# Optimization experiments

Hardware: AMD Instinct MI355X
Metric: run time of the kernel (lower is better)

## Reference

```python
import jax, jax.numpy as jnp
import numpy as np

BN_SCALE = 1.0 / np.sqrt(1.0 + 1e-5)  # eval BatchNorm with running stats (0,1), gamma=1, beta=0


def fps(xyz, npoint):
    """Farthest point sampling. xyz: [B,N,3] -> int32 indices [B,npoint]. First pick is index 0 (as in pointnet2 CUDA)."""
    xyz = jax.lax.stop_gradient(xyz)  # output is integer indices; non-differentiable
    B, N, _ = xyz.shape

    def step(carry, _):
        dist, last = carry
        p = jnp.take_along_axis(xyz, last[:, None, None], axis=1)  # [B,1,3]
        d = jnp.sum((xyz - p) ** 2, axis=-1)                        # [B,N]
        dist = jnp.minimum(dist, d)
        nxt = jnp.argmax(dist, axis=-1).astype(jnp.int32)
        return (dist, nxt), nxt

    dist0 = jnp.full((B, N), 1e10, dtype=jnp.float32)
    first = jnp.zeros((B,), dtype=jnp.int32)
    _, rest = jax.lax.scan(step, (dist0, first), None, length=npoint - 1)  # [npoint-1, B]
    return jnp.concatenate([first[None, :], rest], axis=0).T  # [B, npoint]


def ball_query(xyz, new_xyz, radius, nsample):
    """For each center pick first nsample point indices with squared dist < radius^2; pad with first hit."""
    xyz = jax.lax.stop_gradient(xyz)
    new_xyz = jax.lax.stop_gradient(new_xyz)
    # expanded squared distance avoids materializing [B,S,N,3]
    d2 = (jnp.sum(new_xyz ** 2, -1)[:, :, None] + jnp.sum(xyz ** 2, -1)[:, None, :]
          - 2.0 * jnp.einsum('bsc,bnc->bsn', new_xyz, xyz))  # [B,S,N]
    N = xyz.shape[1]
    key = jnp.where(d2 < radius * radius, jnp.arange(N, dtype=jnp.int32)[None, None, :], N)
    idx = jnp.sort(key, axis=-1)[..., :nsample]          # first hits in index order
    return jnp.where(idx == N, idx[..., :1], idx)        # pad misses with first hit (center is always a hit)


_gather = jax.vmap(lambda p, i: p[i])  # points [N,C], idx [...] -> [..., C], batched over B


def _mlp(h, params):
    # pointwise Conv2d(1x1) + eval-BN + ReLU stack
    for w, b in params:
        h = jax.nn.relu((h @ w + b) * BN_SCALE)
    return h


def _sa(xyz, feats, npoint, nsample, radius, params):
    ci = fps(xyz, npoint)                               # [B,S]
    new_xyz = _gather(xyz, ci)                          # [B,S,3]
    idx = ball_query(xyz, new_xyz, radius, nsample)     # [B,S,K]
    gx = _gather(xyz, idx) - new_xyz[:, :, None, :]     # centered grouped xyz [B,S,K,3]
    h = jnp.concatenate([gx, _gather(feats, idx)], -1)  # [B,S,K,3+C]
    h = _mlp(h, params)
    return new_xyz, jnp.max(h, axis=2)                  # max-pool over neighbors -> [B,S,Cout]


def pointnetpp_forward(x, w1_0, b1_0, w1_1, b1_1, w1_2, b1_2,
                       w2_0, b2_0, w2_1, b2_1, w2_2, b2_2,
                       w3_0, b3_0, w3_1, b3_1, w3_2, b3_2, fc_w, fc_b):
    B0, NO, NP, C = x.shape
    pc = x.reshape(B0 * NO, NP, C)
    xyz, feats = pc[..., :3], pc[..., 3:]
    xyz, feats = _sa(xyz, feats, 32, 32, 0.2, [(w1_0, b1_0), (w1_1, b1_1), (w1_2, b1_2)])
    xyz, feats = _sa(xyz, feats, 16, 32, 0.4, [(w2_0, b2_0), (w2_1, b2_1), (w2_2, b2_2)])
    # group-all SA: no FPS, no centering (pointnet2 GroupAll)
    h = jnp.concatenate([xyz, feats], -1)[:, None]       # [B,1,N,3+C]
    h = _mlp(h, [(w3_0, b3_0), (w3_1, b3_1), (w3_2, b3_2)])
    g = jnp.max(h, axis=2).reshape(h.shape[0], -1)       # [B,768]
    out = g @ fc_w + fc_b                                # final Linear(768,768)
    return out.reshape(B0, NO, -1)                       # dropout = identity (eval / no_grad inference)


def setup_inputs():
    key = jax.random.key(0)
    ks = jax.random.split(key, 16)
    dims = {'w1_0': (6, 64), 'w1_1': (64, 64), 'w1_2': (64, 128),
            'w2_0': (131, 128), 'w2_1': (128, 128), 'w2_2': (128, 256),
            'w3_0': (259, 256), 'w3_1': (256, 512), 'w3_2': (512, 768),
            'fc_w': (768, 768)}
    inp = {'x': jax.random.normal(ks[0], (32, 64, 1024, 6), dtype=jnp.float32)}
    for i, (name, shp) in enumerate(dims.items()):
        inp[name] = 0.05 * jax.random.normal(ks[i + 1], shp, dtype=jnp.float32)
        bname = 'fc_b' if name == 'fc_w' else name.replace('w', 'b', 1)
        inp[bname] = jnp.zeros((shp[1],), dtype=jnp.float32)
    return inp


def reference(x, w1_0, b1_0, w1_1, b1_1, w1_2, b1_2,
              w2_0, b2_0, w2_1, b2_1, w2_2, b2_2,
              w3_0, b3_0, w3_1, b3_1, w3_2, b3_2, fc_w, fc_b):
    return pointnetpp_forward(x, w1_0, b1_0, w1_1, b1_1, w1_2, b1_2,
                              w2_0, b2_0, w2_1, b2_1, w2_2, b2_2,
                              w3_0, b3_0, w3_1, b3_1, w3_2, b3_2, fc_w, fc_b)
```

## Files before the change

### kernel.cpp

```cpp
#include <hip/hip_runtime.h>
#include <math.h>

#define BN_SCALE 0.999995000037499687f
#define NPTS 1024
#define NB   2048

typedef __attribute__((ext_vector_type(8))) short bh8;
typedef __attribute__((ext_vector_type(4))) float f32x4;

__device__ __forceinline__ float sq3(float x, float y, float z) {
  return __fadd_rn(__fadd_rn(__fmul_rn(x, x), __fmul_rn(y, y)), __fmul_rn(z, z));
}

__device__ __forceinline__ short bf16hi(float v) {
  unsigned u = __float_as_uint(v);
  unsigned r = (u + 0x7FFFu + ((u >> 16) & 1u)) >> 16;
  return (short)r;
}
__device__ __forceinline__ float bf16tof(short s) {
  unsigned u = ((unsigned)(unsigned short)s) << 16;
  return __uint_as_float(u);
}
__device__ __forceinline__ void bf16split(float v, short& hi, short& lo) {
  hi = bf16hi(v);
  lo = bf16hi(v - bf16tof(hi));
}

__global__ __launch_bounds__(256) void k_fps1(const float* __restrict__ x,
                                              float* __restrict__ nxyz1) {
  int b = blockIdx.x;
  const float* cloud = x + (size_t)b * NPTS * 6;
  __shared__ float px[NPTS], py[NPTS], pz[NPTS], dist[NPTS];
  __shared__ float wv_s[4];
  __shared__ int   wi_s[4];
  __shared__ int   last_s;
  int t = threadIdx.x;
  for (int i = t; i < NPTS; i += 256) {
    px[i] = cloud[i * 6 + 0];
    py[i] = cloud[i * 6 + 1];
    pz[i] = cloud[i * 6 + 2];
    dist[i] = 1e10f;
  }
  __syncthreads();
  if (t == 0) {
    nxyz1[(size_t)b * 96 + 0] = px[0];
    nxyz1[(size_t)b * 96 + 1] = py[0];
    nxyz1[(size_t)b * 96 + 2] = pz[0];
  }
  int last = 0;
  for (int s = 1; s < 32; ++s) {
    float lx = px[last], ly = py[last], lz = pz[last];
    float bv = -1.0f; int bi = NPTS;
    for (int i = t; i < NPTS; i += 256) {
      float dx = __fsub_rn(px[i], lx);
      float dy = __fsub_rn(py[i], ly);
      float dz = __fsub_rn(pz[i], lz);
      float d  = sq3(dx, dy, dz);
      float nd = fminf(dist[i], d);
      dist[i] = nd;
      if (nd > bv || (nd == bv && i < bi)) { bv = nd; bi = i; }
    }
    for (int off = 32; off; off >>= 1) {
      float ov = __shfl_down(bv, off);
      int   oi = __shfl_down(bi, off);
      if (ov > bv || (ov == bv && oi < bi)) { bv = ov; bi = oi; }
    }
    if ((t & 63) == 0) { wv_s[t >> 6] = bv; wi_s[t >> 6] = bi; }
    __syncthreads();
    if (t == 0) {
      for (int w = 1; w < 4; ++w)
        if (wv_s[w] > bv || (wv_s[w] == bv && wi_s[w] < bi)) { bv = wv_s[w]; bi = wi_s[w]; }
      last_s = bi;
      nxyz1[(size_t)b * 96 + s * 3 + 0] = px[bi];
      nxyz1[(size_t)b * 96 + s * 3 + 1] = py[bi];
      nxyz1[(size_t)b * 96 + s * 3 + 2] = pz[bi];
    }
    __syncthreads();
    last = last_s;
  }
}

__global__ __launch_bounds__(256) void k_bq1(const float* __restrict__ x,
                                             const float* __restrict__ nxyz1,
                                             int* __restrict__ idx1) {
  int c = blockIdx.x * 256 + threadIdx.x;
  if (c >= NB * 32) return;
  int b = c >> 5;
  const float* cloud = x + (size_t)b * NPTS * 6;
  float cx = nxyz1[c * 3 + 0], cy = nxyz1[c * 3 + 1], cz = nxyz1[c * 3 + 2];
  float sqc = sq3(cx, cy, cz);
  const float r2 = (float)(0.2 * 0.2);
  int hits = 0, fh = NPTS - 1;
  int* outp = idx1 + (size_t)c * 32;
  for (int i = 0; i < NPTS; ++i) {
    float ppx = cloud[i * 6 + 0], ppy = cloud[i * 6 + 1], ppz = cloud[i * 6 + 2];
    float sqp = sq3(ppx, ppy, ppz);
    float dt  = __fadd_rn(__fadd_rn(__fmul_rn(cx, ppx), __fmul_rn(cy, ppy)), __fmul_rn(cz, ppz));
    float d2  = __fsub_rn(__fadd_rn(sqc, sqp), __fmul_rn(2.0f, dt));
    if (d2 < r2) {
      if (hits == 0) fh = i;
      outp[hits] = i;
      if (++hits == 32) break;
    }
  }
  for (int j = hits; j < 32; ++j) outp[j] = fh;
}

__device__ __forceinline__ void prep_one(const float* __restrict__ src,
                                         short* __restrict__ dst,
                                         int q, int KT, int Kreal, int N, int permS) {
  int nt = q / (KT * 512);
  int r  = q - nt * (KT * 512);
  int kt = r >> 9;
  int e  = r & 511;
  int l = e >> 3, i = e & 7;
  int k = kt * 32 + ((l >> 4) << 3) + i;
  int col = nt * 16 + (l & 15);
  int ko = k;
  if (permS) ko = (k < permS) ? k + 3 : k - permS;
  float v = (k < Kreal) ? src[(size_t)ko * N + col] : 0.f;
  short hi, lo;
  bf16split(v, hi, lo);
  size_t base = ((size_t)(nt * KT + kt) * 2) * 512 + e;
  dst[base] = hi;
  dst[base + 512] = lo;
}

__global__ __launch_bounds__(256) void k_prep(const float* __restrict__ w0,
                                              const float* __restrict__ w1,
                                              const float* __restrict__ w2,
                                              short* __restrict__ wt0,
                                              short* __restrict__ wt1,
                                              short* __restrict__ wt2) {
  int p = blockIdx.x * 256 + threadIdx.x;
  const int S1 = 8 * 5 * 512, S2 = 8 * 4 * 512, S3 = 16 * 4 * 512;
  if (p < S1)                 prep_one(w0, wt0, p,           5, 131, 128, 128);
  else if (p < S1 + S2)       prep_one(w1, wt1, p - S1,      4, 128, 128, 0);
  else if (p < S1 + S2 + S3)  prep_one(w2, wt2, p - S1 - S2, 4, 128, 256, 0);
}

__global__ __launch_bounds__(256) void k_prep1(const float* __restrict__ w0,
                                               const float* __restrict__ w1,
                                               const float* __restrict__ w2,
                                               short* __restrict__ wt0,
                                               short* __restrict__ wt1,
                                               short* __restrict__ wt2) {
  int p = blockIdx.x * 256 + threadIdx.x;
  const int S1 = 4 * 1 * 512, S2 = 4 * 2 * 512, S3 = 8 * 2 * 512;
  if (p < S1)                 prep_one(w0, wt0, p,           1, 6,  64, 0);
  else if (p < S1 + S2)       prep_one(w1, wt1, p - S1,      2, 64, 64, 0);
  else if (p < S1 + S2 + S3)  prep_one(w2, wt2, p - S1 - S2, 2, 64, 128, 0);
}

__global__ __launch_bounds__(256) void k_prep3(const float* __restrict__ w0,
                                               const float* __restrict__ w1,
                                               const float* __restrict__ w2,
                                               const float* __restrict__ wf,
                                               short* __restrict__ wt0,
                                               short* __restrict__ wt1,
                                               short* __restrict__ wt2,
                                               short* __restrict__ wtf) {
  int p = blockIdx.x * 256 + threadIdx.x;
  const int S1 = 16 * 9 * 512;
  const int S2 = 32 * 8 * 512;
  const int S3 = 48 * 16 * 512;
  const int S4 = 48 * 24 * 512;
  if (p < S1)                      prep_one(w0, wt0, p,                9,  259, 256, 256);
  else if (p < S1 + S2)            prep_one(w1, wt1, p - S1,           8,  256, 512, 0);
  else if (p < S1 + S2 + S3)       prep_one(w2, wt2, p - S1 - S2,      16, 512, 768, 0);
  else if (p < S1 + S2 + S3 + S4)  prep_one(wf, wtf, p - S1 - S2 - S3, 24, 768, 768, 0);
}

template<int NTL, int KT, int PA, int MT>
__device__ __forceinline__ void mfma_gemm(const short* Ahi, const short* Alo,
                                          const short* __restrict__ wt,
                                          int w, int l, int lrow, int lk,
                                          f32x4 acc[][MT]) {
  for (int kt = 0; kt < KT; ++kt) {
    bh8 ahi[MT], alo[MT];
    #pragma unroll
    for (int mt = 0; mt < MT; ++mt) {
      int aoff = (mt * 16 + lrow) * PA + kt * 32 + lk;
      ahi[mt] = *(const bh8*)(Ahi + aoff);
      alo[mt] = *(const bh8*)(Alo + aoff);
    }
    #pragma unroll
    for (int ntl = 0; ntl < NTL; ++ntl) {
      int nt = w * NTL + ntl;
      bh8 bhi = *(const bh8*)(wt + (size_t)((nt * KT + kt) * 2 + 0) * 512 + l * 8);
      bh8 blo = *(const bh8*)(wt + (size_t)((nt * KT + kt) * 2 + 1) * 512 + l * 8);
      #pragma unroll
      for (int mt = 0; mt < MT; ++mt) {
        acc[ntl][mt] = __builtin_amdgcn_mfma_f32_16x16x32_bf16(ahi[mt], bhi, acc[ntl][mt], 0, 0, 0);
        acc[ntl][mt] = __builtin_amdgcn_mfma_f32_16x16x32_bf16(ahi[mt], blo, acc[ntl][mt], 0, 0, 0);
        acc[ntl][mt] = __builtin_amdgcn_mfma_f32_16x16x32_bf16(alo[mt], bhi, acc[ntl][mt], 0, 0, 0);
      }
    }
  }
}

template<int NTL, int PD, int MT>
__device__ __forceinline__ void epi_mid(f32x4 acc[][MT], const float* __restrict__ bias,
                                        short* Dhi, short* Dlo,
                                        int w, int lrow, int lhi4) {
  #pragma unroll
  for (int ntl = 0; ntl < NTL; ++ntl) {
    int col = (w * NTL + ntl) * 16 + lrow;
    float bv = bias[col];
    #pragma unroll
    for (int mt = 0; mt < MT; ++mt) {
      #pragma unroll
      for (int r = 0; r < 4; ++r) {
        int row = mt * 16 + lhi4 + r;
        float o = fmaxf((acc[ntl][mt][r] + bv) * BN_SCALE, 0.f);
        short hi, lo;
        bf16split(o, hi, lo);
        Dhi[row * PD + col] = hi;
        Dlo[row * PD + col] = lo;
      }
    }
  }
}

template<int NTL>
__device__ __forceinline__ void epi_max_bf(f32x4 acc[][4], const float* __restrict__ bias,
                                           short* __restrict__ hiA, short* __restrict__ loA,
                                           short* __restrict__ hiB, short* __restrict__ loB,
                                           int w, int l, int lrow) {
  #pragma unroll
  for (int ntl = 0; ntl < NTL; ++ntl) {
    int col = (w * NTL + ntl) * 16 + lrow;
    float bv = bias[col];
    float m0 = 0.f, m1 = 0.f;
    #pragma unroll
    for (int mt = 0; mt < 4; ++mt) {
      float mm = 0.f;
      #pragma unroll
      for (int r = 0; r < 4; ++r)
        mm = fmaxf(mm, fmaxf((acc[ntl][mt][r] + bv) * BN_SCALE, 0.f));
      if (mt < 2) m0 = fmaxf(m0, mm); else m1 = fmaxf(m1, mm);
    }
    m0 = fmaxf(m0, __shfl_xor(m0, 16)); m0 = fmaxf(m0, __shfl_xor(m0, 32));
    m1 = fmaxf(m1, __shfl_xor(m1, 16)); m1 = fmaxf(m1, __shfl_xor(m1, 32));
    if (l < 16) {
      short hi, lo;
      bf16split(m0, hi, lo); hiA[col] = hi; loA[col] = lo;
      bf16split(m1, hi, lo); hiB[col] = hi; loB[col] = lo;
    }
  }
}

__global__ __launch_bounds__(256) void k_sa1(const float* __restrict__ x,
                                             const float* __restrict__ nxyz1,
                                             const int* __restrict__ idx1,
                                             const short* __restrict__ wt0,
                                             const short* __restrict__ wt1,
                                             const short* __restrict__ wt2,
                                             const float* __restrict__ b0g,
                                             const float* __restrict__ b1g,
                                             const float* __restrict__ b2g,
                                             short* __restrict__ f1hi,
                                             short* __restrict__ f1lo) {
  int c2 = blockIdx.x;
  int t  = threadIdx.x;
  __shared__ __align__(16) short lds[18432];
  __shared__ int pts[64];
  short* h0hi = lds;
  short* h0lo = lds + 4608;
  short* h1hi = lds + 9216;
  short* h1lo = lds + 13824;
  short* h2hi = lds;
  short* h2lo = lds + 4608;

  if (t < 64) {
    int g = t >> 5, samp = t & 31;
    pts[t] = idx1[(size_t)(c2 * 2 + g) * 32 + samp];
  }
  for (int j = t; j < 64 * 34; j += 256) {
    int s = j / 34, d = 6 + (j - s * 34);
    h0hi[s * 40 + d] = 0;
    h0lo[s * 40 + d] = 0;
  }
  __syncthreads();

  for (int j = t; j < 384; j += 256) {
    int s = j / 6, d = j - (j / 6) * 6;
    int g = s >> 5; int c = c2 * 2 + g; int b = c >> 5;
    int pt = pts[s];
    float v = x[((size_t)b * NPTS + pt) * 6 + d];
    if (d < 3) v -= nxyz1[(size_t)c * 3 + d];
    short hi, lo; bf16split(v, hi, lo);
    h0hi[s * 40 + d] = hi; h0lo[s * 40 + d] = lo;
  }
  __syncthreads();

  int l = t & 63, w = t >> 6;
  int lrow = l & 15;
  int lk   = (l >> 4) << 3;
  int lhi4 = (l >> 4) << 2;
  f32x4 zz = {0.f, 0.f, 0.f, 0.f};

  {
    f32x4 acc[1][4];
    #pragma unroll
    for (int j = 0; j < 4; ++j) acc[0][j] = zz;
    mfma_gemm<1, 1, 40, 4>(h0hi, h0lo, wt0, w, l, lrow, lk, acc);
    epi_mid<1, 72, 4>(acc, b0g, h1hi, h1lo, w, lrow, lhi4);
  }
  __syncthreads();
  {
    f32x4 acc[1][4];
    #pragma unroll
    for (int j = 0; j < 4; ++j) acc[0][j] = zz;
    mfma_gemm<1, 2, 72, 4>(h1hi, h1lo, wt1, w, l, lrow, lk, acc);
    epi_mid<1, 72, 4>(acc, b1g, h2hi, h2lo, w, lrow, lhi4);
  }
  __syncthreads();
  {
    f32x4 acc[2][4];
    #pragma unroll
    for (int i = 0; i < 2; ++i)
      #pragma unroll
      for (int j = 0; j < 4; ++j) acc[i][j] = zz;
    mfma_gemm<2, 2, 72, 4>(h2hi, h2lo, wt2, w, l, lrow, lk, acc);
    epi_max_bf<2>(acc, b2g,
                  f1hi + (size_t)(c2 * 2 + 0) * 128, f1lo + (size_t)(c2 * 2 + 0) * 128,
                  f1hi + (size_t)(c2 * 2 + 1) * 128, f1lo + (size_t)(c2 * 2 + 1) * 128,
                  w, l, lrow);
  }
}

__global__ __launch_bounds__(64) void k_fps2(const float* __restrict__ nxyz1,
                                             float* __restrict__ nxyz2) {
  int b = blockIdx.x;
  int t = threadIdx.x;
  const float* pts = nxyz1 + (size_t)b * 96;
  float ppx = 0.f, ppy = 0.f, ppz = 0.f, dist = -1.f;
  if (t < 32) { ppx = pts[t * 3]; ppy = pts[t * 3 + 1]; ppz = pts[t * 3 + 2]; dist = 1e10f; }
  if (t == 0) {
    nxyz2[(size_t)b * 48 + 0] = ppx;
    nxyz2[(size_t)b * 48 + 1] = ppy;
    nxyz2[(size_t)b * 48 + 2] = ppz;
  }
  int last = 0;
  for (int s = 1; s < 16; ++s) {
    float lx = __shfl(ppx, last), ly = __shfl(ppy, last), lz = __shfl(ppz, last);
    if (t < 32) {
      float dx = __fsub_rn(ppx, lx);
      float dy = __fsub_rn(ppy, ly);
      float dz = __fsub_rn(ppz, lz);
      dist = fminf(dist, sq3(dx, dy, dz));
    }
    float bv = dist; int bi = (t < 32) ? t : 1000;
    for (int off = 32; off; off >>= 1) {
      float ov = __shfl_xor(bv, off);
      int   oi = __shfl_xor(bi, off);
      if (ov > bv || (ov == bv && oi < bi)) { bv = ov; bi = oi; }
    }
    last = bi;
    float bx = __shfl(ppx, last), by = __shfl(ppy, last), bz = __shfl(ppz, last);
    if (t == 0) {
      nxyz2[(size_t)b * 48 + s * 3 + 0] = bx;
      nxyz2[(size_t)b * 48 + s * 3 + 1] = by;
      nxyz2[(size_t)b * 48 + s * 3 + 2] = bz;
    }
  }
}

__global__ __launch_bounds__(256) void k_bq2(const float* __restrict__ nxyz1,
                                             const float* __restrict__ nxyz2,
                                             int* __restrict__ idx2) {
  int c = blockIdx.x * 256 + threadIdx.x;
  if (c >= NB * 16) return;
  int b = c >> 4;
  const float* pts = nxyz1 + (size_t)b * 96;
  float cx = nxyz2[c * 3 + 0], cy = nxyz2[c * 3 + 1], cz = nxyz2[c * 3 + 2];
  float sqc = sq3(cx, cy, cz);
  const float r2 = (float)(0.4 * 0.4);
  int hits = 0, fh = 31;
  int* outp = idx2 + (size_t)c * 32;
  for (int i = 0; i < 32; ++i) {
    float ppx = pts[i * 3], ppy = pts[i * 3 + 1], ppz = pts[i * 3 + 2];
    float sqp = sq3(ppx, ppy, ppz);
    float dt  = __fadd_rn(__fadd_rn(__fmul_rn(cx, ppx), __fmul_rn(cy, ppy)), __fmul_rn(cz, ppz));
    float d2  = __fsub_rn(__fadd_rn(sqc, sqp), __fmul_rn(2.0f, dt));
    if (d2 < r2) { if (hits == 0) fh = i; outp[hits++] = i; }
  }
  for (int j = hits; j < 32; ++j) outp[j] = fh;
}

__global__ __launch_bounds__(512, 4) void k_sa2(const float* __restrict__ nxyz1,
                                                const float* __restrict__ nxyz2,
                                                const int* __restrict__ idx2,
                                                const short* __restrict__ f1hi,
                                                const short* __restrict__ f1lo,
                                                const short* __restrict__ wt0,
                                                const short* __restrict__ wt1,
                                                const short* __restrict__ wt2,
                                                const float* __restrict__ b0g,
                                                const float* __restrict__ b1g,
                                                const float* __restrict__ b2g,
                                                short* __restrict__ f2hi,
                                                short* __restrict__ f2lo) {
  int c2 = blockIdx.x;
  int t  = threadIdx.x;
  __shared__ __align__(16) short lds[38912];
  __shared__ int pts[64];
  short* h0hi = lds;
  short* h0lo = lds + 10752;
  short* h1hi = lds + 21504;
  short* h1lo = lds + 30208;
  short* h2hi = lds;
  short* h2lo = lds + 10752;

  if (t < 64) {
    int g = t >> 5, samp = t & 31;
    pts[t] = idx2[(size_t)(c2 * 2 + g) * 32 + samp];
  }
  for (int j = t; j < 64 * 29; j += 512) {
    int s = j / 29, d = 131 + (j - s * 29);
    h0hi[s * 168 + d] = 0;
    h0lo[s * 168 + d] = 0;
  }
  __syncthreads();

  for (int j = t; j < 1024; j += 512) {
    int s = j >> 4, c8 = j & 15;
    int g = s >> 5; int c = c2 * 2 + g; int b = c >> 4;
    int pt = pts[s];
    size_t src = ((size_t)b * 32 + pt) * 128 + c8 * 8;
    *(bh8*)(h0hi + s * 168 + c8 * 8) = *(const bh8*)(f1hi + src);
    *(bh8*)(h0lo + s * 168 + c8 * 8) = *(const bh8*)(f1lo + src);
  }
  for (int j = t; j < 192; j += 512) {
    int s = j / 3, d = j - (j / 3) * 3;
    int g = s >> 5; int c = c2 * 2 + g; int b = c >> 4;
    int pt = pts[s];
    float v = nxyz1[((size_t)b * 32 + pt) * 3 + d] - nxyz2[(size_t)c * 3 + d];
    short hi, lo; bf16split(v, hi, lo);
    h0hi[s * 168 + 128 + d] = hi; h0lo[s * 168 + 128 + d] = lo;
  }
  __syncthreads();

  int l = t & 63, w = t >> 6;
  int lrow = l & 15;
  int lk   = (l >> 4) << 3;
  int lhi4 = (l >> 4) << 2;
  f32x4 zz = {0.f, 0.f, 0.f, 0.f};

  {
    f32x4 acc[1][4];
    #pragma unroll
    for (int j = 0; j < 4; ++j) acc[0][j] = zz;
    mfma_gemm<1, 5, 168, 4>(h0hi, h0lo, wt0, w, l, lrow, lk, acc);
    epi_mid<1, 136, 4>(acc, b0g, h1hi, h1lo, w, lrow, lhi4);
  }
  __syncthreads();
  {
    f32x4 acc[1][4];
    #pragma unroll
    for (int j = 0; j < 4; ++j) acc[0][j] = zz;
    mfma_gemm<1, 4, 136, 4>(h1hi, h1lo, wt1, w, l, lrow, lk, acc);
    epi_mid<1, 136, 4>(acc, b1g, h2hi, h2lo, w, lrow, lhi4);
  }
  __syncthreads();
  {
    f32x4 acc[2][4];
    #pragma unroll
    for (int i = 0; i < 2; ++i)
      #pragma unroll
      for (int j = 0; j < 4; ++j) acc[i][j] = zz;
    mfma_gemm<2, 4, 136, 4>(h2hi, h2lo, wt2, w, l, lrow, lk, acc);
    epi_max_bf<2>(acc, b2g,
                  f2hi + (size_t)(c2 * 2 + 0) * 256, f2lo + (size_t)(c2 * 2 + 0) * 256,
                  f2hi + (size_t)(c2 * 2 + 1) * 256, f2lo + (size_t)(c2 * 2 + 1) * 256,
                  w, l, lrow);
  }
}

__global__ __launch_bounds__(256) void k_mlp3(const float* __restrict__ nxyz2,
                                              const short* __restrict__ f2hi,
                                              const short* __restrict__ f2lo,
                                              const short* __restrict__ wt0,
                                              const short* __restrict__ wt1,
                                              const short* __restrict__ wt2,
                                              const float* __restrict__ b0g,
                                              const float* __restrict__ b1g,
                                              const float* __restrict__ b2g,
                                              short* __restrict__ ghi,
                                              short* __restrict__ glo) {
  int b = blockIdx.x;
  int t = threadIdx.x;
  __shared__ __align__(16) short lds[25088];
  short* h1hi = lds;
  short* h1lo = lds + 4224;
  short* h0hi = lds + 8448;
  short* h0lo = lds + 13184;
  short* h2hi = lds + 8448;
  short* h2lo = lds + 16768;

  for (int j = t; j < 16 * 29; j += 256) {
    int s = j / 29, d = 259 + (j - s * 29);
    h0hi[s * 296 + d] = 0;
    h0lo[s * 296 + d] = 0;
  }
  for (int j = t; j < 512; j += 256) {
    int s = j >> 5, c8 = j & 31;
    size_t src = ((size_t)b * 16 + s) * 256 + c8 * 8;
    *(bh8*)(h0hi + s * 296 + c8 * 8) = *(const bh8*)(f2hi + src);
    *(bh8*)(h0lo + s * 296 + c8 * 8) = *(const bh8*)(f2lo + src);
  }
  for (int j = t; j < 48; j += 256) {
    int s = j / 3, d = j - (j / 3) * 3;
    float v = nxyz2[(size_t)b * 48 + s * 3 + d];
    short hi, lo; bf16split(v, hi, lo);
    h0hi[s * 296 + 256 + d] = hi;
    h0lo[s * 296 + 256 + d] = lo;
  }
  __syncthreads();

  int l = t & 63, w = t >> 6;
  int lrow = l & 15;
  int lk   = (l >> 4) << 3;
  int lhi4 = (l >> 4) << 2;
  f32x4 zz = {0.f, 0.f, 0.f, 0.f};

  {
    f32x4 acc[4][1];
    #pragma unroll
    for (int i = 0; i < 4; ++i) acc[i][0] = zz;
    mfma_gemm<4, 9, 296, 1>(h0hi, h0lo, wt0, w, l, lrow, lk, acc);
    epi_mid<4, 264, 1>(acc, b0g, h1hi, h1lo, w, lrow, lhi4);
  }
  __syncthreads();
  {
    f32x4 acc[8][1];
    #pragma unroll
    for (int i = 0; i < 8; ++i) acc[i][0] = zz;
    mfma_gemm<8, 8, 264, 1>(h1hi, h1lo, wt1, w, l, lrow, lk, acc);
    epi_mid<8, 520, 1>(acc, b1g, h2hi, h2lo, w, lrow, lhi4);
  }
  __syncthreads();
  {
    f32x4 acc[12][1];
    #pragma unroll
    for (int i = 0; i < 12; ++i) acc[i][0] = zz;
    mfma_gemm<12, 16, 520, 1>(h2hi, h2lo, wt2, w, l, lrow, lk, acc);
    #pragma unroll
    for (int ntl = 0; ntl < 12; ++ntl) {
      int col = (w * 12 + ntl) * 16 + lrow;
      float bv = b2g[col];
      float m = 0.f;
      #pragma unroll
      for (int r = 0; r < 4; ++r)
        m = fmaxf(m, fmaxf((acc[ntl][0][r] + bv) * BN_SCALE, 0.f));
      m = fmaxf(m, __shfl_xor(m, 16));
      m = fmaxf(m, __shfl_xor(m, 32));
      if (l < 16) {
        short hi, lo; bf16split(m, hi, lo);
        ghi[(size_t)b * 768 + col] = hi;
        glo[(size_t)b * 768 + col] = lo;
      }
    }
  }
}

__global__ __launch_bounds__(256) void k_fc(const short* __restrict__ ghi,
                                            const short* __restrict__ glo,
                                            const short* __restrict__ wtf,
                                            const float* __restrict__ fcb,
                                            float* __restrict__ outp) {
  int mblk = blockIdx.x;
  int nh   = blockIdx.y;
  int t = threadIdx.x;
  int l = t & 63, w = t >> 6;
  int lrow = l & 15;
  int lk   = (l >> 4) << 3;
  int lhi4 = (l >> 4) << 2;
  f32x4 zz = {0.f, 0.f, 0.f, 0.f};

  const short* Ahi = ghi + (size_t)mblk * 16 * 768;
  const short* Alo = glo + (size_t)mblk * 16 * 768;
  const short* wt  = wtf + (size_t)nh * 24 * 24 * 1024;

  f32x4 acc[6][1];
  #pragma unroll
  for (int i = 0; i < 6; ++i) acc[i][0] = zz;
  mfma_gemm<6, 24, 768, 1>(Ahi, Alo, wt, w, l, lrow, lk, acc);

  #pragma unroll
  for (int ntl = 0; ntl < 6; ++ntl) {
    int col = nh * 384 + (w * 6 + ntl) * 16 + lrow;
    float bv = fcb[col];
    #pragma unroll
    for (int r = 0; r < 4; ++r) {
      int row = mblk * 16 + lhi4 + r;
      outp[(size_t)row * 768 + col] = acc[ntl][0][r] + bv;
    }
  }
}

extern "C" void kernel_launch(void* const* d_in, const int* in_sizes, int n_in,
                              void* d_out, int out_size, void* d_ws, size_t ws_size,
                              hipStream_t stream) {
  const float* x    = (const float*)d_in[0];
  const float* w1_0 = (const float*)d_in[1];  const float* b1_0 = (const float*)d_in[2];
  const float* w1_1 = (const float*)d_in[3];  const float* b1_1 = (const float*)d_in[4];
  const float* w1_2 = (const float*)d_in[5];  const float* b1_2 = (const float*)d_in[6];
  const float* w2_0 = (const float*)d_in[7];  const float* b2_0 = (const float*)d_in[8];
  const float* w2_1 = (const float*)d_in[9];  const float* b2_1 = (const float*)d_in[10];
  const float* w2_2 = (const float*)d_in[11]; const float* b2_2 = (const float*)d_in[12];
  const float* w3_0 = (const float*)d_in[13]; const float* b3_0 = (const float*)d_in[14];
  const float* w3_1 = (const float*)d_in[15]; const float* b3_1 = (const float*)d_in[16];
  const float* w3_2 = (const float*)d_in[17]; const float* b3_2 = (const float*)d_in[18];
  const float* fc_w = (const float*)d_in[19]; const float* fc_b = (const float*)d_in[20];
  float* outp = (float*)d_out;

  const size_t n_float = (size_t)NB * 96 + (size_t)NB * 48;
  const size_t n_int   = (size_t)NB * 1024 + (size_t)NB * 512;
  const size_t n_short = 4 * (size_t)NB * 4096
                       + (40960 + 32768 + 65536)
                       + (4096 + 8192 + 16384)
                       + (147456 + 262144 + 786432) + 1179648
                       + 2 * (size_t)NB * 768;
  const size_t need_bytes = n_float * 4 + n_int * 4 + n_short * 2;
  if (ws_size < need_bytes) return;

  float* nxyz1 = (float*)d_ws;
  float* nxyz2 = nxyz1 + (size_t)NB * 96;
  int*   idx1  = (int*)(nxyz2 + (size_t)NB * 48);
  int*   idx2  = idx1 + (size_t)NB * 1024;
  short* f1hi  = (short*)(idx2 + (size_t)NB * 512);
  short* f1lo  = f1hi + (size_t)NB * 4096;
  short* f2hi  = f1lo + (size_t)NB * 4096;
  short* f2lo  = f2hi + (size_t)NB * 4096;
  short* wt0   = f2lo + (size_t)NB * 4096;
  short* wt1   = wt0 + 40960;
  short* wt2   = wt1 + 32768;
  short* wt10  = wt2 + 65536;
  short* wt11  = wt10 + 4096;
  short* wt12  = wt11 + 8192;
  short* wt30  = wt12 + 16384;
  short* wt31  = wt30 + 147456;
  short* wt32  = wt31 + 262144;
  short* wtfc  = wt32 + 786432;
  short* ghi   = wtfc + 1179648;
  short* glo   = ghi + (size_t)NB * 768;

  k_prep <<<272, 256, 0, stream>>>(w2_0, w2_1, w2_2, wt0, wt1, wt2);
  k_prep1<<<56, 256, 0, stream>>>(w1_0, w1_1, w1_2, wt10, wt11, wt12);
  k_prep3<<<4640, 256, 0, stream>>>(w3_0, w3_1, w3_2, fc_w, wt30, wt31, wt32, wtfc);
  k_fps1<<<NB, 256, 0, stream>>>(x, nxyz1);
  k_bq1 <<<(NB * 32) / 256, 256, 0, stream>>>(x, nxyz1, idx1);
  k_sa1 <<<NB * 16, 256, 0, stream>>>(x, nxyz1, idx1, wt10, wt11, wt12,
                                      b1_0, b1_1, b1_2, f1hi, f1lo);
  k_fps2<<<NB, 64, 0, stream>>>(nxyz1, nxyz2);
  k_bq2 <<<(NB * 16) / 256, 256, 0, stream>>>(nxyz1, nxyz2, idx2);
  k_sa2 <<<NB * 8, 512, 0, stream>>>(nxyz1, nxyz2, idx2, f1hi, f1lo,
                                     wt0, wt1, wt2, b2_0, b2_1, b2_2, f2hi, f2lo);
  k_mlp3<<<NB, 256, 0, stream>>>(nxyz2, f2hi, f2lo, wt30, wt31, wt32,
                                 b3_0, b3_1, b3_2, ghi, glo);
  k_fc  <<<dim3(NB / 16, 2), 256, 0, stream>>>(ghi, glo, wtfc, fc_b, outp);
}
```

Measured before the change: 1.286 ms.

## Retile MFMA warp work into 2x2 M/N groups and batch two clouds in mlp3

The MFMA GEMM helper now takes separate M-group and N-group indices. In sa1 and sa2 each wave covers two M tiles and several N tiles instead of four M tiles and one N tile, which rebalances how A fragments from LDS and B fragments from global memory are reused. k_mlp3 now processes two batch items per 512-thread block with MT=2, so each weight fragment loaded from global memory is used for two rows of tiles, roughly halving weight traffic. The cost is double the LDS per block and more accumulator registers, which may lower occupancy.

```diff
diff --git a/kernel.cpp b/kernel.cpp
--- a/kernel.cpp
+++ b/kernel.cpp
@@ -171,22 +171,22 @@
   else if (p < S1 + S2 + S3 + S4)  prep_one(wf, wtf, p - S1 - S2 - S3, 24, 768, 768, 0);
 }
 
-template<int NTL, int KT, int PA, int MT>
+template<int MT, int NTL, int KT, int PA>
 __device__ __forceinline__ void mfma_gemm(const short* Ahi, const short* Alo,
                                           const short* __restrict__ wt,
-                                          int w, int l, int lrow, int lk,
+                                          int mg, int ng, int l, int lrow, int lk,
                                           f32x4 acc[][MT]) {
   for (int kt = 0; kt < KT; ++kt) {
     bh8 ahi[MT], alo[MT];
     #pragma unroll
     for (int mt = 0; mt < MT; ++mt) {
-      int aoff = (mt * 16 + lrow) * PA + kt * 32 + lk;
+      int aoff = ((mg * MT + mt) * 16 + lrow) * PA + kt * 32 + lk;
       ahi[mt] = *(const bh8*)(Ahi + aoff);
       alo[mt] = *(const bh8*)(Alo + aoff);
     }
     #pragma unroll
     for (int ntl = 0; ntl < NTL; ++ntl) {
-      int nt = w * NTL + ntl;
+      int nt = ng * NTL + ntl;
       bh8 bhi = *(const bh8*)(wt + (size_t)((nt * KT + kt) * 2 + 0) * 512 + l * 8);
       bh8 blo = *(const bh8*)(wt + (size_t)((nt * KT + kt) * 2 + 1) * 512 + l * 8);
       #pragma unroll
@@ -199,19 +199,19 @@
   }
 }
 
-template<int NTL, int PD, int MT>
+template<int MT, int NTL, int PD>
 __device__ __forceinline__ void epi_mid(f32x4 acc[][MT], const float* __restrict__ bias,
                                         short* Dhi, short* Dlo,
-                                        int w, int lrow, int lhi4) {
+                                        int mg, int ng, int lrow, int lhi4) {
   #pragma unroll
   for (int ntl = 0; ntl < NTL; ++ntl) {
-    int col = (w * NTL + ntl) * 16 + lrow;
+    int col = (ng * NTL + ntl) * 16 + lrow;
     float bv = bias[col];
     #pragma unroll
     for (int mt = 0; mt < MT; ++mt) {
       #pragma unroll
       for (int r = 0; r < 4; ++r) {
-        int row = mt * 16 + lhi4 + r;
+        int row = (mg * MT + mt) * 16 + lhi4 + r;
         float o = fmaxf((acc[ntl][mt][r] + bv) * BN_SCALE, 0.f);
         short hi, lo;
         bf16split(o, hi, lo);
@@ -222,30 +222,25 @@
   }
 }
 
-template<int NTL>
-__device__ __forceinline__ void epi_max_bf(f32x4 acc[][4], const float* __restrict__ bias,
-                                           short* __restrict__ hiA, short* __restrict__ loA,
-                                           short* __restrict__ hiB, short* __restrict__ loB,
-                                           int w, int l, int lrow) {
+template<int MT, int NTL>
+__device__ __forceinline__ void epi_max_bf(f32x4 acc[][MT], const float* __restrict__ bias,
+                                           short* __restrict__ hiC, short* __restrict__ loC,
+                                           int ng, int l, int lrow) {
   #pragma unroll
   for (int ntl = 0; ntl < NTL; ++ntl) {
-    int col = (w * NTL + ntl) * 16 + lrow;
+    int col = (ng * NTL + ntl) * 16 + lrow;
     float bv = bias[col];
-    float m0 = 0.f, m1 = 0.f;
-    #pragma unroll
-    for (int mt = 0; mt < 4; ++mt) {
-      float mm = 0.f;
+    float m = 0.f;
+    #pragma unroll
+    for (int mt = 0; mt < MT; ++mt)
       #pragma unroll
       for (int r = 0; r < 4; ++r)
-        mm = fmaxf(mm, fmaxf((acc[ntl][mt][r] + bv) * BN_SCALE, 0.f));
-      if (mt < 2) m0 = fmaxf(m0, mm); else m1 = fmaxf(m1, mm);
-    }
-    m0 = fmaxf(m0, __shfl_xor(m0, 16)); m0 = fmaxf(m0, __shfl_xor(m0, 32));
-    m1 = fmaxf(m1, __shfl_xor(m1, 16)); m1 = fmaxf(m1, __shfl_xor(m1, 32));
+        m = fmaxf(m, fmaxf((acc[ntl][mt][r] + bv) * BN_SCALE, 0.f));
+    m = fmaxf(m, __shfl_xor(m, 16));
+    m = fmaxf(m, __shfl_xor(m, 32));
     if (l < 16) {
-      short hi, lo;
-      bf16split(m0, hi, lo); hiA[col] = hi; loA[col] = lo;
-      bf16split(m1, hi, lo); hiB[col] = hi; loB[col] = lo;
+      short hi, lo; bf16split(m, hi, lo);
+      hiC[col] = hi; loC[col] = lo;
     }
   }
 }
@@ -295,38 +290,37 @@
   __syncthreads();
 
   int l = t & 63, w = t >> 6;
+  int mg = w & 1, ng = w >> 1;
   int lrow = l & 15;
   int lk   = (l >> 4) << 3;
   int lhi4 = (l >> 4) << 2;
   f32x4 zz = {0.f, 0.f, 0.f, 0.f};
 
   {
-    f32x4 acc[1][4];
-    #pragma unroll
-    for (int j = 0; j < 4; ++j) acc[0][j] = zz;
-    mfma_gemm<1, 1, 40, 4>(h0hi, h0lo, wt0, w, l, lrow, lk, acc);
-    epi_mid<1, 72, 4>(acc, b0g, h1hi, h1lo, w, lrow, lhi4);
-  }
-  __syncthreads();
-  {
-    f32x4 acc[1][4];
-    #pragma unroll
-    for (int j = 0; j < 4; ++j) acc[0][j] = zz;
-    mfma_gemm<1, 2, 72, 4>(h1hi, h1lo, wt1, w, l, lrow, lk, acc);
-    epi_mid<1, 72, 4>(acc, b1g, h2hi, h2lo, w, lrow, lhi4);
-  }
-  __syncthreads();
-  {
-    f32x4 acc[2][4];
-    #pragma unroll
-    for (int i = 0; i < 2; ++i)
-      #pragma unroll
-      for (int j = 0; j < 4; ++j) acc[i][j] = zz;
-    mfma_gemm<2, 2, 72, 4>(h2hi, h2lo, wt2, w, l, lrow, lk, acc);
-    epi_max_bf<2>(acc, b2g,
-                  f1hi + (size_t)(c2 * 2 + 0) * 128, f1lo + (size_t)(c2 * 2 + 0) * 128,
-                  f1hi + (size_t)(c2 * 2 + 1) * 128, f1lo + (size_t)(c2 * 2 + 1) * 128,
-                  w, l, lrow);
+    f32x4 acc[2][2];
+    #pragma unroll
+    for (int i = 0; i < 2; ++i) { acc[i][0] = zz; acc[i][1] = zz; }
+    mfma_gemm<2, 2, 1, 40>(h0hi, h0lo, wt0, mg, ng, l, lrow, lk, acc);
+    epi_mid<2, 2, 72>(acc, b0g, h1hi, h1lo, mg, ng, lrow, lhi4);
+  }
+  __syncthreads();
+  {
+    f32x4 acc[2][2];
+    #pragma unroll
+    for (int i = 0; i < 2; ++i) { acc[i][0] = zz; acc[i][1] = zz; }
+    mfma_gemm<2, 2, 2, 72>(h1hi, h1lo, wt1, mg, ng, l, lrow, lk, acc);
+    epi_mid<2, 2, 72>(acc, b1g, h2hi, h2lo, mg, ng, lrow, lhi4);
+  }
+  __syncthreads();
+  {
+    f32x4 acc[4][2];
+    #pragma unroll
+    for (int i = 0; i < 4; ++i) { acc[i][0] = zz; acc[i][1] = zz; }
+    mfma_gemm<2, 4, 2, 72>(h2hi, h2lo, wt2, mg, ng, l, lrow, lk, acc);
+    epi_max_bf<2, 4>(acc, b2g,
+                     f1hi + (size_t)(c2 * 2 + mg) * 128,
+                     f1lo + (size_t)(c2 * 2 + mg) * 128,
+                     ng, l, lrow);
   }
 }
 
@@ -443,42 +437,41 @@
   __syncthreads();
 
   int l = t & 63, w = t >> 6;
+  int mg = w & 1, ng = w >> 1;
   int lrow = l & 15;
   int lk   = (l >> 4) << 3;
   int lhi4 = (l >> 4) << 2;
   f32x4 zz = {0.f, 0.f, 0.f, 0.f};
 
   {
-    f32x4 acc[1][4];
-    #pragma unroll
-    for (int j = 0; j < 4; ++j) acc[0][j] = zz;
-    mfma_gemm<1, 5, 168, 4>(h0hi, h0lo, wt0, w, l, lrow, lk, acc);
-    epi_mid<1, 136, 4>(acc, b0g, h1hi, h1lo, w, lrow, lhi4);
-  }
-  __syncthreads();
-  {
-    f32x4 acc[1][4];
-    #pragma unroll
-    for (int j = 0; j < 4; ++j) acc[0][j] = zz;
-    mfma_gemm<1, 4, 136, 4>(h1hi, h1lo, wt1, w, l, lrow, lk, acc);
-    epi_mid<1, 136, 4>(acc, b1g, h2hi, h2lo, w, lrow, lhi4);
-  }
-  __syncthreads();
-  {
-    f32x4 acc[2][4];
-    #pragma unroll
-    for (int i = 0; i < 2; ++i)
-      #pragma unroll
-      for (int j = 0; j < 4; ++j) acc[i][j] = zz;
-    mfma_gemm<2, 4, 136, 4>(h2hi, h2lo, wt2, w, l, lrow, lk, acc);
-    epi_max_bf<2>(acc, b2g,
-                  f2hi + (size_t)(c2 * 2 + 0) * 256, f2lo + (size_t)(c2 * 2 + 0) * 256,
-                  f2hi + (size_t)(c2 * 2 + 1) * 256, f2lo + (size_t)(c2 * 2 + 1) * 256,
-                  w, l, lrow);
-  }
-}
-
-__global__ __launch_bounds__(256) void k_mlp3(const float* __restrict__ nxyz2,
+    f32x4 acc[2][2];
+    #pragma unroll
+    for (int i = 0; i < 2; ++i) { acc[i][0] = zz; acc[i][1] = zz; }
+    mfma_gemm<2, 2, 5, 168>(h0hi, h0lo, wt0, mg, ng, l, lrow, lk, acc);
+    epi_mid<2, 2, 136>(acc, b0g, h1hi, h1lo, mg, ng, lrow, lhi4);
+  }
+  __syncthreads();
+  {
+    f32x4 acc[2][2];
+    #pragma unroll
+    for (int i = 0; i < 2; ++i) { acc[i][0] = zz; acc[i][1] = zz; }
+    mfma_gemm<2, 2, 4, 136>(h1hi, h1lo, wt1, mg, ng, l, lrow, lk, acc);
+    epi_mid<2, 2, 136>(acc, b1g, h2hi, h2lo, mg, ng, lrow, lhi4);
+  }
+  __syncthreads();
+  {
+    f32x4 acc[4][2];
+    #pragma unroll
+    for (int i = 0; i < 4; ++i) { acc[i][0] = zz; acc[i][1] = zz; }
+    mfma_gemm<2, 4, 4, 136>(h2hi, h2lo, wt2, mg, ng, l, lrow, lk, acc);
+    epi_max_bf<2, 4>(acc, b2g,
+                     f2hi + (size_t)(c2 * 2 + mg) * 256,
+                     f2lo + (size_t)(c2 * 2 + mg) * 256,
+                     ng, l, lrow);
+  }
+}
+
+__global__ __launch_bounds__(512) void k_mlp3(const float* __restrict__ nxyz2,
                                               const short* __restrict__ f2hi,
                                               const short* __restrict__ f2lo,
                                               const short* __restrict__ wt0,
@@ -489,30 +482,32 @@
                                               const float* __restrict__ b2g,
                                               short* __restrict__ ghi,
                                               short* __restrict__ glo) {
-  int b = blockIdx.x;
+  int b2 = blockIdx.x;
   int t = threadIdx.x;
-  __shared__ __align__(16) short lds[25088];
+  __shared__ __align__(16) short lds[50176];
   short* h1hi = lds;
-  short* h1lo = lds + 4224;
-  short* h0hi = lds + 8448;
-  short* h0lo = lds + 13184;
-  short* h2hi = lds + 8448;
-  short* h2lo = lds + 16768;
-
-  for (int j = t; j < 16 * 29; j += 256) {
+  short* h1lo = lds + 8448;
+  short* h0hi = lds + 16896;
+  short* h0lo = lds + 26368;
+  short* h2hi = lds + 16896;
+  short* h2lo = lds + 33536;
+
+  for (int j = t; j < 32 * 29; j += 512) {
     int s = j / 29, d = 259 + (j - s * 29);
     h0hi[s * 296 + d] = 0;
     h0lo[s * 296 + d] = 0;
   }
-  for (int j = t; j < 512; j += 256) {
+  for (int j = t; j < 1024; j += 512) {
     int s = j >> 5, c8 = j & 31;
-    size_t src = ((size_t)b * 16 + s) * 256 + c8 * 8;
+    int cl = b2 * 2 + (s >> 4);
+    size_t src = ((size_t)cl * 16 + (s & 15)) * 256 + c8 * 8;
     *(bh8*)(h0hi + s * 296 + c8 * 8) = *(const bh8*)(f2hi + src);
     *(bh8*)(h0lo + s * 296 + c8 * 8) = *(const bh8*)(f2lo + src);
   }
-  for (int j = t; j < 48; j += 256) {
+  for (int j = t; j < 96; j += 512) {
     int s = j / 3, d = j - (j / 3) * 3;
-    float v = nxyz2[(size_t)b * 48 + s * 3 + d];
+    int cl = b2 * 2 + (s >> 4);
+    float v = nxyz2[(size_t)cl * 48 + (s & 15) * 3 + d];
     short hi, lo; bf16split(v, hi, lo);
     h0hi[s * 296 + 256 + d] = hi;
     h0lo[s * 296 + 256 + d] = lo;
@@ -526,40 +521,43 @@
   f32x4 zz = {0.f, 0.f, 0.f, 0.f};
 
   {
-    f32x4 acc[4][1];
-    #pragma unroll
-    for (int i = 0; i < 4; ++i) acc[i][0] = zz;
-    mfma_gemm<4, 9, 296, 1>(h0hi, h0lo, wt0, w, l, lrow, lk, acc);
-    epi_mid<4, 264, 1>(acc, b0g, h1hi, h1lo, w, lrow, lhi4);
-  }
-  __syncthreads();
-  {
-    f32x4 acc[8][1];
-    #pragma unroll
-    for (int i = 0; i < 8; ++i) acc[i][0] = zz;
-    mfma_gemm<8, 8, 264, 1>(h1hi, h1lo, wt1, w, l, lrow, lk, acc);
-    epi_mid<8, 520, 1>(acc, b1g, h2hi, h2lo, w, lrow, lhi4);
-  }
-  __syncthreads();
-  {
-    f32x4 acc[12][1];
-    #pragma unroll
-    for (int i = 0; i < 12; ++i) acc[i][0] = zz;
-    mfma_gemm<12, 16, 520, 1>(h2hi, h2lo, wt2, w, l, lrow, lk, acc);
-    #pragma unroll
-    for (int ntl = 0; ntl < 12; ++ntl) {
-      int col = (w * 12 + ntl) * 16 + lrow;
+    f32x4 acc[2][2];
+    #pragma unroll
+    for (int i = 0; i < 2; ++i) { acc[i][0] = zz; acc[i][1] = zz; }
+    mfma_gemm<2, 2, 9, 296>(h0hi, h0lo, wt0, 0, w, l, lrow, lk, acc);
+    epi_mid<2, 2, 264>(acc, b0g, h1hi, h1lo, 0, w, lrow, lhi4);
+  }
+  __syncthreads();
+  {
+    f32x4 acc[4][2];
+    #pragma unroll
+    for (int i = 0; i < 4; ++i) { acc[i][0] = zz; acc[i][1] = zz; }
+    mfma_gemm<2, 4, 8, 264>(h1hi, h1lo, wt1, 0, w, l, lrow, lk, acc);
+    epi_mid<2, 4, 520>(acc, b1g, h2hi, h2lo, 0, w, lrow, lhi4);
+  }
+  __syncthreads();
+  {
+    f32x4 acc[6][2];
+    #pragma unroll
+    for (int i = 0; i < 6; ++i) { acc[i][0] = zz; acc[i][1] = zz; }
+    mfma_gemm<2, 6, 16, 520>(h2hi, h2lo, wt2, 0, w, l, lrow, lk, acc);
+    #pragma unroll
+    for (int ntl = 0; ntl < 6; ++ntl) {
+      int col = (w * 6 + ntl) * 16 + lrow;
       float bv = b2g[col];
-      float m = 0.f;
       #pragma unroll
-      for (int r = 0; r < 4; ++r)
-        m = fmaxf(m, fmaxf((acc[ntl][0][r] + bv) * BN_SCALE, 0.f));
-      m = fmaxf(m, __shfl_xor(m, 16));
-      m = fmaxf(m, __shfl_xor(m, 32));
-      if (l < 16) {
-        short hi, lo; bf16split(m, hi, lo);
-        ghi[(size_t)b * 768 + col] = hi;
-        glo[(size_t)b * 768 + col] = lo;
+      for (int mt = 0; mt < 2; ++mt) {
+        float m = 0.f;
+        #pragma unroll
+        for (int r = 0; r < 4; ++r)
+          m = fmaxf(m, fmaxf((acc[ntl][mt][r] + bv) * BN_SCALE, 0.f));
+        m = fmaxf(m, __shfl_xor(m, 16));
+        m = fmaxf(m, __shfl_xor(m, 32));
+        if (l < 16) {
+          short hi, lo; bf16split(m, hi, lo);
+          ghi[(size_t)(b2 * 2 + mt) * 768 + col] = hi;
+          glo[(size_t)(b2 * 2 + mt) * 768 + col] = lo;
+        }
       }
     }
   }
@@ -586,7 +584,7 @@
   f32x4 acc[6][1];
   #pragma unroll
   for (int i = 0; i < 6; ++i) acc[i][0] = zz;
-  mfma_gemm<6, 24, 768, 1>(Ahi, Alo, wt, w, l, lrow, lk, acc);
+  mfma_gemm<1, 6, 24, 768>(Ahi, Alo, wt, 0, w, l, lrow, lk, acc);
 
   #pragma unroll
   for (int ntl = 0; ntl < 6; ++ntl) {
@@ -658,7 +656,7 @@
   k_bq2 <<<(NB * 16) / 256, 256, 0, stream>>>(nxyz1, nxyz2, idx2);
   k_sa2 <<<NB * 8, 512, 0, stream>>>(nxyz1, nxyz2, idx2, f1hi, f1lo,
                                      wt0, wt1, wt2, b2_0, b2_1, b2_2, f2hi, f2lo);
-  k_mlp3<<<NB, 256, 0, stream>>>(nxyz2, f2hi, f2lo, wt30, wt31, wt32,
-                                 b3_0, b3_1, b3_2, ghi, glo);
+  k_mlp3<<<NB / 2, 512, 0, stream>>>(nxyz2, f2hi, f2lo, wt30, wt31, wt32,
+                                     b3_0, b3_1, b3_2, ghi, glo);
   k_fc  <<<dim3(NB / 16, 2), 256, 0, stream>>>(ghi, glo, wtfc, fc_b, outp);
 }
```

Measured after the change: 1.245 ms. 1.03x faster.
